# Kernel optimization log

Hardware: AMD Instinct MI355X
Metric: run time of the kernel (lower is better)

## Reference

```python
import jax, jax.numpy as jnp
import numpy as np
import math

D_MODEL = 1024
N_HEADS = 16
D_KV = 64
NUM_BUCKETS = 32
MAX_DISTANCE = 128
BATCH = 4
SEQ = 2048


def _relative_position_bucket(relative_position, num_buckets=NUM_BUCKETS, max_distance=MAX_DISTANCE):
    # bidirectional=True (encoder)
    num_buckets //= 2
    relative_buckets = (relative_position > 0).astype(jnp.int32) * num_buckets
    rp = jnp.abs(relative_position)
    max_exact = num_buckets // 2
    is_small = rp < max_exact
    rp_safe = jnp.maximum(rp, 1)  # avoid log(0); masked by is_small anyway
    rp_if_large = max_exact + (
        jnp.log(rp_safe.astype(jnp.float32) / max_exact)
        / math.log(max_distance / max_exact)
        * (num_buckets - max_exact)
    ).astype(jnp.int32)
    rp_if_large = jnp.minimum(rp_if_large, num_buckets - 1)
    relative_buckets += jnp.where(is_small, rp, rp_if_large)
    return relative_buckets


def compute_bias(rel_bias, q_len, k_len):
    context = jnp.arange(q_len)[:, None]
    memory = jnp.arange(k_len)[None, :]
    buckets = _relative_position_bucket(memory - context)  # [q, k]
    values = rel_bias[buckets]                              # [q, k, h]
    return jnp.transpose(values, (2, 0, 1))[None]           # [1, h, q, k]


def setup_inputs() -> dict:
    key = jax.random.key(0)
    ks = jax.random.split(key, 6)
    s = 1.0 / math.sqrt(D_MODEL)
    return {
        "hidden_states": jax.random.normal(ks[0], (BATCH, SEQ, D_MODEL), jnp.float32),
        "wq": jax.random.normal(ks[1], (D_MODEL, N_HEADS * D_KV), jnp.float32) * s,
        "wk": jax.random.normal(ks[2], (D_MODEL, N_HEADS * D_KV), jnp.float32) * s,
        "wv": jax.random.normal(ks[3], (D_MODEL, N_HEADS * D_KV), jnp.float32) * s,
        "wo": jax.random.normal(ks[4], (N_HEADS * D_KV, D_MODEL), jnp.float32) * s,
        "rel_bias": jax.random.normal(ks[5], (NUM_BUCKETS, N_HEADS), jnp.float32) * 0.5,
    }


def reference(hidden_states, wq, wk, wv, wo, rel_bias):
    B, S, _ = hidden_states.shape

    def shape(x):  # [B,S,H*Dk] -> [B,H,S,Dk]
        return x.reshape(B, S, N_HEADS, D_KV).transpose(0, 2, 1, 3)

    q = shape(hidden_states @ wq)
    k = shape(hidden_states @ wk)
    v = shape(hidden_states @ wv)

    # NOTE: T5 does NOT scale by 1/sqrt(d_kv)
    scores = jnp.einsum("bhqd,bhkd->bhqk", q, k)
    position_bias = compute_bias(rel_bias, S, S)  # [1,H,S,S]
    scores = scores + position_bias
    attn = jax.nn.softmax(scores.astype(jnp.float32), axis=-1).astype(scores.dtype)
    ctx = jnp.einsum("bhqk,bhkd->bhqd", attn, v)
    ctx = ctx.transpose(0, 2, 1, 3).reshape(B, S, N_HEADS * D_KV)
    return ctx @ wo
```

## Files before the change

kernel.cpp:

```cpp
#include <hip/hip_runtime.h>
#include <hip/hip_bf16.h>

typedef unsigned short u16;
typedef unsigned int   u32;
typedef __bf16 bf16x8 __attribute__((ext_vector_type(8)));
typedef __bf16 bf16x4 __attribute__((ext_vector_type(4)));
typedef short  s16x4  __attribute__((ext_vector_type(4)));
typedef float  f32x4  __attribute__((ext_vector_type(4)));
typedef u16    u16x8  __attribute__((ext_vector_type(8)));
typedef u16    u16x4  __attribute__((ext_vector_type(4)));
typedef u32    u32x2  __attribute__((ext_vector_type(2)));

#define MFMA16(a,b,c) __builtin_amdgcn_mfma_f32_16x16x32_bf16(a,b,c,0,0,0)
#define LOG2E 1.4426950408889634f

__device__ __forceinline__ f32x4 mfma16k16(bf16x4 a, bf16x4 b, f32x4 c) {
#if __has_builtin(__builtin_amdgcn_mfma_f32_16x16x16bf16_1k)
    return __builtin_amdgcn_mfma_f32_16x16x16bf16_1k(
        __builtin_bit_cast(s16x4, a), __builtin_bit_cast(s16x4, b), c, 0, 0, 0);
#elif __has_builtin(__builtin_amdgcn_mfma_f32_16x16x16_bf16_1k)
    return __builtin_amdgcn_mfma_f32_16x16x16_bf16_1k(
        __builtin_bit_cast(s16x4, a), __builtin_bit_cast(s16x4, b), c, 0, 0, 0);
#else
    asm("v_mfma_f32_16x16x16_bf16 %0, %1, %2, %0" : "+v"(c) : "v"(a), "v"(b));
    return c;
#endif
}

__device__ __forceinline__ u16 f2b(float f) {
    u32 u = __builtin_bit_cast(u32, f);
    u32 r = (u + 0x7FFFu + ((u >> 16) & 1u)) >> 16;
    return (u16)r;
}

typedef const __attribute__((address_space(1))) u32* gaddr_t;
typedef __attribute__((address_space(3))) u32*       laddr_t;
__device__ __forceinline__ void gl_lds16(const void* g, void* l) {
    __builtin_amdgcn_global_load_lds((gaddr_t)g, (laddr_t)l, 16, 0, 0);
}

__global__ __launch_bounds__(256) void prep_kernel(
        const float* __restrict__ H, const float* __restrict__ wq,
        const float* __restrict__ wk, const float* __restrict__ wv,
        const float* __restrict__ wo, const float* __restrict__ rel_bias,
        u16* __restrict__ Hb, u16* __restrict__ Wt, u16* __restrict__ Wot,
        float* __restrict__ tab) {
    __shared__ u16 tile[64 * 72];
    int bi = blockIdx.x;
    int t = threadIdx.x;
    if (bi < 4096) {
        int i = (bi * 256 + t) * 8;
        float4 a = *(const float4*)(H + i);
        float4 b = *(const float4*)(H + i + 4);
        u16x8 o = { f2b(a.x), f2b(a.y), f2b(a.z), f2b(a.w),
                    f2b(b.x), f2b(b.y), f2b(b.z), f2b(b.w) };
        *(u16x8*)(Hb + i) = o;
    } else if (bi < 5120) {
        int g2 = bi - 4096;
        int g = g2 >> 8, rem = g2 & 255;
        int n0 = (rem >> 4) * 64, k0 = (rem & 15) * 64;
        const float* src = (g == 0) ? wq : (g == 1) ? wk : (g == 2) ? wv : wo;
        u16* dst = (g < 3) ? (Wt + g * 1048576) : Wot;
#pragma unroll
        for (int rr = 0; rr < 4; ++rr) {
            int idx = rr * 256 + t;
            int kr = idx >> 4, c = idx & 15;
            float4 v = *(const float4*)(src + (k0 + kr) * 1024 + n0 + c * 4);
            u16x4 o = { f2b(v.x), f2b(v.y), f2b(v.z), f2b(v.w) };
            *(u16x4*)&tile[kr * 72 + c * 4] = o;
        }
        __syncthreads();
#pragma unroll
        for (int rr = 0; rr < 2; ++rr) {
            int idx = rr * 256 + t;
            int n = idx >> 3, c = idx & 7;
            u16x8 o;
#pragma unroll
            for (int j = 0; j < 8; ++j) o[j] = tile[(c * 8 + j) * 72 + n];
            *(u16x8*)(dst + (n0 + n) * 1024 + k0 + c * 8) = o;
        }
    } else {
        int i = (bi - 5120) * 256 + t;
        int h = i >> 12;
        int idx = i & 4095;
        int delta = idx - 2048;
        int bucket = (delta > 0) ? 16 : 0;
        int rp = delta < 0 ? -delta : delta;
        if (rp < 8) {
            bucket += rp;
        } else {
            double v = log((double)rp / 8.0) / log(16.0) * 8.0;
            int tt = (int)v;
            int b2 = 8 + tt;
            bucket += (b2 < 15) ? b2 : 15;
        }
        tab[h * 4096 + idx] = rel_bias[bucket * 16 + h] * LOG2E;
    }
}

template <int MODE>
__global__ __launch_bounds__(256) void gemm_bt(
        const u16* __restrict__ A, const u16* __restrict__ Bt, int K, int N,
        u16* __restrict__ q_out, u16* __restrict__ k_out, u16* __restrict__ v_out,
        float* __restrict__ f_out) {
    __shared__ u16 As[128 * 32];
    __shared__ u16 Bs[128 * 32];
    __shared__ u16 vt_tile[MODE == 0 ? 128 * 136 : 1];
    int t = threadIdx.x;
    int lane = t & 63, w = t >> 6;
    int wm = w & 1, wn = w >> 1;
    int ln = lane & 15, quad = lane >> 4;
    int m0 = blockIdx.x * 128, n0 = blockIdx.y * 128;
    const u16* Ab = A + m0 * K;
    const u16* Bb = Bt + n0 * K;
    f32x4 acc[4][4] = {};
    int nk = K >> 5;
    for (int kt = 0; kt < nk; ++kt) {
        int k0 = kt * 32;
#pragma unroll
        for (int rr = 0; rr < 2; ++rr) {
            int idx = rr * 256 + t;
            int row = idx >> 2, c = (idx & 3) ^ (row & 3);
            gl_lds16(Ab + row * K + k0 + c * 8, ((char*)As) + idx * 16);
            gl_lds16(Bb + row * K + k0 + c * 8, ((char*)Bs) + idx * 16);
        }
        __syncthreads();
        bf16x8 af[4], bfr[4];
#pragma unroll
        for (int mb = 0; mb < 4; ++mb) {
            int row = wm * 64 + mb * 16 + ln;
            af[mb] = *(const bf16x8*)&As[row * 32 + ((quad ^ (row & 3)) << 3)];
        }
#pragma unroll
        for (int nb = 0; nb < 4; ++nb) {
            int row = wn * 64 + nb * 16 + ln;
            bfr[nb] = *(const bf16x8*)&Bs[row * 32 + ((quad ^ (row & 3)) << 3)];
        }
#pragma unroll
        for (int mb = 0; mb < 4; ++mb)
#pragma unroll
            for (int nb = 0; nb < 4; ++nb)
                acc[mb][nb] = MFMA16(af[mb], bfr[nb], acc[mb][nb]);
        __syncthreads();
    }
    if (MODE == 0 && n0 >= 2048) {
#pragma unroll
        for (int mb = 0; mb < 4; ++mb)
#pragma unroll
            for (int nb = 0; nb < 4; ++nb)
#pragma unroll
                for (int r = 0; r < 4; ++r) {
                    int np = wn * 64 + nb * 16 + ln;
                    int mp = wm * 64 + mb * 16 + quad * 4 + r;
                    vt_tile[np * 136 + mp] = f2b(acc[mb][nb][r]);
                }
        __syncthreads();
        int h0 = (n0 >> 6) & 15;
        int b = m0 >> 11;
        int s0 = m0 & 2047;
#pragma unroll
        for (int j = 0; j < 8; ++j) {
            int e = j * 256 + t;
            int d_all = e >> 4;
            int sc = e & 15;
            int hh = h0 + (d_all >> 6);
            int d = d_all & 63;
            u16x8 val = *(const u16x8*)&vt_tile[d_all * 136 + sc * 8];
            *(u16x8*)(v_out + (b * 16 + hh) * 131072 + d * 2048 + s0 + sc * 8) = val;
        }
    } else {
#pragma unroll
        for (int mb = 0; mb < 4; ++mb)
#pragma unroll
            for (int nb = 0; nb < 4; ++nb)
#pragma unroll
                for (int r = 0; r < 4; ++r) {
                    int m = m0 + wm * 64 + mb * 16 + quad * 4 + r;
                    int n = n0 + wn * 64 + nb * 16 + ln;
                    float v = acc[mb][nb][r];
                    if (MODE == 0) {
                        int which = n >> 10, h = (n >> 6) & 15, d = n & 63;
                        int b = m >> 11, s = m & 2047;
                        u16* dst = (which == 0) ? q_out : k_out;
                        float scale = (which == 0) ? LOG2E : 1.0f;
                        dst[(((b << 4) + h) * 2048 + s) * 64 + d] = f2b(v * scale);
                    } else {
                        f_out[m * N + n] = v;
                    }
                }
    }
}

__global__ __launch_bounds__(256, 4) void attn_kernel(
        const u16* __restrict__ Qb, const u16* __restrict__ Kb,
        const u16* __restrict__ Vt, const float* __restrict__ bias_tab,
        u16* __restrict__ ctx) {
    __shared__ u16 Ks[2][64 * 64];
    __shared__ u16 Vs[2][64 * 64];
    __shared__ float sb[384];
    int t = threadIdx.x;
    int lane = t & 63, w = t >> 6;
    int ln = lane & 15, quad = lane >> 4;
    int bid = blockIdx.x;
    int bh = (bid & 7) * 8 + (bid >> 7);
    int qtile = (bid >> 3) & 15;
    int h = bh & 15, b = bh >> 4;
    int q0 = qtile * 128;

    float chi = bias_tab[h * 4096 + 2048 + 1500];
    float clo = bias_tab[h * 4096 + 2048 - 1500];

    const float* tb = bias_tab + h * 4096 + 1857;
    for (int i = t; i < 384; i += 256) sb[i] = tb[i];

    const u16* qbase = Qb + (bh * 2048 + q0 + w * 16 + ln) * 64 + quad * 8;
    bf16x8 qf[2][2];
    qf[0][0] = *(const bf16x8*)(qbase);
    qf[0][1] = *(const bf16x8*)(qbase + 32);
    qf[1][0] = *(const bf16x8*)(qbase + 64 * 64);
    qf[1][1] = *(const bf16x8*)(qbase + 64 * 64 + 32);

    const u16* Kbase = Kb + bh * 2048 * 64;
    const u16* Vbase = Vt + bh * 64 * 2048;

    f32x4 oacc[2][4] = {};
    float l0 = 0.0f, l1 = 0.0f;
    int cb2_base = 191 - w * 16 + quad * 4 - ln;

    auto stage = [&](int kb, int bufidx) {
#pragma unroll
        for (int it = 0; it < 2; ++it) {
            int idx = it * 256 + t;
            int row = idx >> 3, c = (idx & 7) ^ (row & 7);
            gl_lds16(Kbase + (kb + row) * 64 + c * 8,
                     ((char*)&Ks[bufidx][0]) + idx * 16);
            gl_lds16(Vbase + row * 2048 + kb + c * 8,
                     ((char*)&Vs[bufidx][0]) + idx * 16);
        }
    };

    auto compute = [&](int kb0, const u16* Kc, const u16* Vc) {
        f32x4 sacc[2][4];
        int diffs[2] = {kb0 - q0, kb0 - q0 - 64};
        __builtin_amdgcn_s_setprio(1);
#pragma unroll
        for (int nb = 0; nb < 4; ++nb) {
            int key = nb * 16 + ln;
            int sw = key & 7;
            bf16x8 kf0 = *(const bf16x8*)&Kc[key * 64 + ((quad ^ sw) << 3)];
            bf16x8 kf1 = *(const bf16x8*)&Kc[key * 64 + (((quad ^ 4) ^ sw) << 3)];
#pragma unroll
            for (int g = 0; g < 2; ++g) {
                int diff = diffs[g];
                f32x4 ci;
                if (diff >= 192 || diff <= -192) {
                    float c0 = (diff > 0) ? chi : clo;
                    ci = {c0, c0, c0, c0};
                } else {
                    const float* bp = &sb[diff + cb2_base + nb * 16];
                    ci = {bp[0], bp[1], bp[2], bp[3]};
                }
                f32x4 scc = MFMA16(kf0, qf[g][0], ci);
                sacc[g][nb] = MFMA16(kf1, qf[g][1], scc);
            }
        }
        __builtin_amdgcn_s_setprio(0);

        bf16x4 pb[2][4];
#pragma unroll
        for (int g = 0; g < 2; ++g) {
            float s0 = 0.f, s1 = 0.f, s2 = 0.f, s3 = 0.f;
#pragma unroll
            for (int nb = 0; nb < 4; ++nb) {
                float e0 = __builtin_amdgcn_exp2f(sacc[g][nb][0]);
                float e1 = __builtin_amdgcn_exp2f(sacc[g][nb][1]);
                float e2 = __builtin_amdgcn_exp2f(sacc[g][nb][2]);
                float e3 = __builtin_amdgcn_exp2f(sacc[g][nb][3]);
                s0 += e0; s1 += e1; s2 += e2; s3 += e3;
                u32 lo, hi;
                asm("v_cvt_pk_bf16_f32 %0, %1, %2" : "=v"(lo) : "v"(e0), "v"(e1));
                asm("v_cvt_pk_bf16_f32 %0, %1, %2" : "=v"(hi) : "v"(e2), "v"(e3));
                u32x2 uv = {lo, hi};
                pb[g][nb] = __builtin_bit_cast(bf16x4, uv);
            }
            if (g == 0) l0 += (s0 + s1) + (s2 + s3);
            else        l1 += (s0 + s1) + (s2 + s3);
        }

        __builtin_amdgcn_s_setprio(1);
#pragma unroll
        for (int kc = 0; kc < 4; ++kc) {
            bf16x4 vA[4];
#pragma unroll
            for (int nd = 0; nd < 4; ++nd) {
                int d = nd * 16 + ln;
                int ch = (kc * 2 + (quad >> 1)) ^ (d & 7);
                vA[nd] = *(const bf16x4*)&Vc[d * 64 + (ch << 3) + ((quad & 1) << 2)];
            }
#pragma unroll
            for (int nd = 0; nd < 4; ++nd)
#pragma unroll
                for (int g = 0; g < 2; ++g)
                    oacc[g][nd] = mfma16k16(vA[nd], pb[g][kc], oacc[g][nd]);
        }
        __builtin_amdgcn_s_setprio(0);
    };

    stage(0, 0);
    asm volatile("s_waitcnt lgkmcnt(0)" ::: "memory");
    for (int kt = 0; kt < 31; ++kt) {
        int cur = kt & 1;
        stage((kt + 1) * 64, cur ^ 1);
        asm volatile("s_waitcnt vmcnt(4)" ::: "memory");
        __builtin_amdgcn_sched_barrier(0);
        __builtin_amdgcn_s_barrier();
        compute(kt * 64, &Ks[cur][0], &Vs[cur][0]);
        __builtin_amdgcn_s_barrier();
    }
    asm volatile("s_waitcnt vmcnt(0)" ::: "memory");
    __builtin_amdgcn_sched_barrier(0);
    __builtin_amdgcn_s_barrier();
    compute(31 * 64, &Ks[1][0], &Vs[1][0]);

    l0 += __shfl_xor(l0, 16); l0 += __shfl_xor(l0, 32);
    l1 += __shfl_xor(l1, 16); l1 += __shfl_xor(l1, 32);
    float linv[2] = {1.0f / l0, 1.0f / l1};
#pragma unroll
    for (int g = 0; g < 2; ++g) {
        int q = q0 + g * 64 + w * 16 + ln;
        u16* cp = ctx + (b * 2048 + q) * 1024 + h * 64 + quad * 4;
#pragma unroll
        for (int nd = 0; nd < 4; ++nd) {
            u16x4 o = { f2b(oacc[g][nd][0] * linv[g]), f2b(oacc[g][nd][1] * linv[g]),
                        f2b(oacc[g][nd][2] * linv[g]), f2b(oacc[g][nd][3] * linv[g]) };
            *(u16x4*)(cp + nd * 16) = o;
        }
    }
}

extern "C" void kernel_launch(void* const* d_in, const int* in_sizes, int n_in,
                              void* d_out, int out_size, void* d_ws, size_t ws_size,
                              hipStream_t stream) {
    const float* H   = (const float*)d_in[0];
    const float* wq  = (const float*)d_in[1];
    const float* wk  = (const float*)d_in[2];
    const float* wv  = (const float*)d_in[3];
    const float* wo  = (const float*)d_in[4];
    const float* rel = (const float*)d_in[5];
    float* out = (float*)d_out;

    char* ws = (char*)d_ws;
    u16* Hb    = (u16*)(ws);
    u16* Wt    = (u16*)(ws + 16777216);
    u16* Wot   = (u16*)(ws + 23068672);
    u16* Qb    = (u16*)(ws + 25165824);
    u16* Kb    = (u16*)(ws + 41943040);
    u16* Vt    = (u16*)(ws + 58720256);
    float* bias_tab = (float*)(ws + 75497472);
    u16* ctx = Hb;

    prep_kernel<<<5376, 256, 0, stream>>>(H, wq, wk, wv, wo, rel, Hb, Wt, Wot, bias_tab);
    gemm_bt<0><<<dim3(64, 24), 256, 0, stream>>>(Hb, Wt, 1024, 3072, Qb, Kb, Vt, nullptr);
    attn_kernel<<<1024, 256, 0, stream>>>(Qb, Kb, Vt, bias_tab, ctx);
    gemm_bt<1><<<dim3(64, 8), 256, 0, stream>>>(ctx, Wot, 1024, 1024, nullptr, nullptr, nullptr, out);
}
```

Measured before the change: 290.8 us.

## Add 256x256-tile 8-wave QKV GEMM with half-K staged LDS pipeline

Adds a new QKV projection kernel that uses 256x256 output tiles with 512 threads and 128KB of dynamic LDS. K tiles are staged into four slots in half-k chunks by direct global-to-LDS loads, and the loads are interleaved with MFMA phases under explicit waitcnt and barrier control. The V output is transposed through LDS so it can be written as vectorised stores. The aim is more operand reuse per loaded byte and better overlap of loads with MFMA than the old 128x128 GEMM. In exchange, occupancy is lower and register pressure is high, since each thread holds 32 accumulators.

Result: slower. 302.9 us (+4.2%).

```diff
diff --git a/kernel.cpp b/kernel.cpp
--- a/kernel.cpp
+++ b/kernel.cpp
@@ -191,6 +191,144 @@
     }
 }
 
+__global__ __launch_bounds__(512, 2) void gemm8_qkv(
+        const u16* __restrict__ A, const u16* __restrict__ Bt, int K,
+        u16* __restrict__ q_out, u16* __restrict__ k_out, u16* __restrict__ v_out) {
+    extern __shared__ u16 pool[];
+    int tid = threadIdx.x;
+    int lane = tid & 63, w = tid >> 6;
+    int wm = w >> 2, wn = w & 3;
+    int ln = lane & 15, quad = lane >> 4;
+    int bid = (int)blockIdx.x;
+    int swz = (bid & 7) * 48 + (bid >> 3);
+    int bx = swz / 12, by = swz - 12 * bx;
+    int m0 = bx * 256, n0 = by * 256;
+    const u16* Ab = A + m0 * K;
+    const u16* Bb = Bt + n0 * K;
+    int NT = K >> 6;
+
+    f32x4 acc[8][4] = {};
+
+    auto stageH = [&](int mat, int slot, int ktile, int kh) {
+        const u16* g = mat ? Bb : Ab;
+        char* ldsb = (char*)(pool + mat * 32768 + slot * 8192);
+        int kb = ktile * 64 + kh * 32;
+#pragma unroll
+        for (int it = 0; it < 2; ++it) {
+            int i = it * 512 + tid;
+            int row = i >> 2;
+            int c = (i & 3) ^ ((row ^ (row >> 2)) & 3);
+            gl_lds16(g + row * K + kb + c * 8, ldsb + i * 16);
+        }
+    };
+    auto ldA = [&](int slot, int r) -> bf16x8 {
+        return *(const bf16x8*)&pool[slot * 8192 + r * 32 +
+                                     ((quad ^ ((r ^ (r >> 2)) & 3)) << 3)];
+    };
+    auto ldB = [&](int slot, int r) -> bf16x8 {
+        return *(const bf16x8*)&pool[32768 + slot * 8192 + r * 32 +
+                                     ((quad ^ ((r ^ (r >> 2)) & 3)) << 3)];
+    };
+
+    stageH(0, 0, 0, 0); stageH(1, 0, 0, 0);
+    stageH(0, 1, 0, 1); stageH(1, 1, 0, 1);
+    if (NT > 1) { stageH(0, 2, 1, 0); stageH(1, 2, 1, 0); }
+    asm volatile("s_waitcnt vmcnt(4)" ::: "memory");
+    __builtin_amdgcn_sched_barrier(0);
+    __builtin_amdgcn_s_barrier();
+    __builtin_amdgcn_sched_barrier(0);
+
+    for (int t = 0; t < NT; ++t) {
+        int p = t & 1;
+#pragma unroll
+        for (int q = 0; q < 4; ++q) {
+            int kk = q >> 1, nh = q & 1;
+            int rs = 2 * p + kk;
+            bf16x8 af[8], bfr[2];
+#pragma unroll
+            for (int mf = 0; mf < 8; ++mf)
+                af[mf] = ldA(rs, wm * 128 + mf * 16 + ln);
+#pragma unroll
+            for (int j = 0; j < 2; ++j)
+                bfr[j] = ldB(rs, wn * 64 + (nh * 2 + j) * 16 + ln);
+            if (q == 0)      { if (t + 1 < NT) stageH(0, 2 * (1 - p) + 1, t + 1, 1); }
+            else if (q == 1) { if (t + 1 < NT) stageH(1, 2 * (1 - p) + 1, t + 1, 1); }
+            else if (q == 2) { if (t + 2 < NT) stageH(0, 2 * p, t + 2, 0); }
+            else             { if (t + 2 < NT) stageH(1, 2 * p, t + 2, 0); }
+            __builtin_amdgcn_s_barrier();
+            __builtin_amdgcn_sched_barrier(0);
+            __builtin_amdgcn_s_setprio(1);
+#pragma unroll
+            for (int mf = 0; mf < 8; ++mf)
+#pragma unroll
+                for (int j = 0; j < 2; ++j)
+                    acc[mf][nh * 2 + j] = MFMA16(af[mf], bfr[j], acc[mf][nh * 2 + j]);
+            __builtin_amdgcn_s_setprio(0);
+            if (q == 3) {
+                if (t >= NT - 3) { asm volatile("s_waitcnt vmcnt(0)" ::: "memory"); }
+                else             { asm volatile("s_waitcnt vmcnt(4)" ::: "memory"); }
+                __builtin_amdgcn_sched_barrier(0);
+            }
+            __builtin_amdgcn_s_barrier();
+            __builtin_amdgcn_sched_barrier(0);
+        }
+    }
+
+    int which = n0 >> 10;
+    if (which < 2) {
+        u16* dst = which ? k_out : q_out;
+        float scale = which ? 1.0f : LOG2E;
+#pragma unroll
+        for (int mf = 0; mf < 8; ++mf) {
+            int m = m0 + wm * 128 + mf * 16 + quad * 4;
+            int bb = m >> 11, s = m & 2047;
+#pragma unroll
+            for (int nf = 0; nf < 4; ++nf) {
+                int n = n0 + wn * 64 + nf * 16 + ln;
+                int h = (n >> 6) & 15, d = n & 63;
+                u16* dp = dst + (((bb << 4) + h) * 2048 + s) * 64 + d;
+#pragma unroll
+                for (int r = 0; r < 4; ++r)
+                    dp[r * 64] = f2b(acc[mf][nf][r] * scale);
+            }
+        }
+    } else {
+        int bb = m0 >> 11, s0 = m0 & 2047;
+#pragma unroll
+        for (int pass = 0; pass < 2; ++pass) {
+            if ((wn >> 1) == pass) {
+#pragma unroll
+                for (int mf = 0; mf < 8; ++mf)
+#pragma unroll
+                    for (int nf = 0; nf < 4; ++nf) {
+                        int npl = (wn & 1) * 64 + nf * 16 + ln;
+                        int mp = wm * 128 + mf * 16 + quad * 4;
+#pragma unroll
+                        for (int r = 0; r < 4; ++r)
+                            pool[npl * 264 + mp + r] = f2b(acc[mf][nf][r]);
+                    }
+            }
+            asm volatile("s_waitcnt lgkmcnt(0)" ::: "memory");
+            __builtin_amdgcn_sched_barrier(0);
+            __builtin_amdgcn_s_barrier();
+            __builtin_amdgcn_sched_barrier(0);
+#pragma unroll
+            for (int j = 0; j < 8; ++j) {
+                int e = j * 512 + tid;
+                int d_all = e >> 5, mc = e & 31;
+                u16x8 val = *(const u16x8*)&pool[d_all * 264 + mc * 8];
+                int n_v = (n0 - 2048) + pass * 128 + d_all;
+                int hh = n_v >> 6, d = n_v & 63;
+                *(u16x8*)(v_out + (bb * 16 + hh) * 131072 + d * 2048 + s0 + mc * 8) = val;
+            }
+            if (pass == 0) {
+                __builtin_amdgcn_s_barrier();
+                __builtin_amdgcn_sched_barrier(0);
+            }
+        }
+    }
+}
+
 __global__ __launch_bounds__(256, 4) void attn_kernel(
         const u16* __restrict__ Qb, const u16* __restrict__ Kb,
         const u16* __restrict__ Vt, const float* __restrict__ bias_tab,
@@ -359,8 +497,19 @@
     float* bias_tab = (float*)(ws + 75497472);
     u16* ctx = Hb;
 
+    static int dyn_ok = -1;
+    if (dyn_ok < 0) {
+        dyn_ok = (hipFuncSetAttribute((const void*)gemm8_qkv,
+                      hipFuncAttributeMaxDynamicSharedMemorySize, 131072)
+                  == hipSuccess) ? 1 : 0;
+    }
+
     prep_kernel<<<5376, 256, 0, stream>>>(H, wq, wk, wv, wo, rel, Hb, Wt, Wot, bias_tab);
-    gemm_bt<0><<<dim3(64, 24), 256, 0, stream>>>(Hb, Wt, 1024, 3072, Qb, Kb, Vt, nullptr);
+    if (dyn_ok) {
+        gemm8_qkv<<<384, 512, 131072, stream>>>(Hb, Wt, 1024, Qb, Kb, Vt);
+    } else {
+        gemm_bt<0><<<dim3(64, 24), 256, 0, stream>>>(Hb, Wt, 1024, 3072, Qb, Kb, Vt, nullptr);
+    }
     attn_kernel<<<1024, 256, 0, stream>>>(Qb, Kb, Vt, bias_tab, ctx);
     gemm_bt<1><<<dim3(64, 8), 256, 0, stream>>>(ctx, Wot, 1024, 1024, nullptr, nullptr, nullptr, out);
 }
```
